# Performance work log

Hardware: AMD Instinct MI355X
Metric: run time of the kernel (lower is better)

Reference implementation:

```python
import jax, jax.numpy as jnp
import numpy as np
from jax import lax


def _na_indices(size, k):
    # NATTEN-style window: window shifts to stay inside the volume.
    centers = np.arange(size)
    start = np.clip(centers - k // 2, 0, size - k)
    idx = start[:, None] + np.arange(k)[None, :]          # (size, k) neighbor coords
    rel = idx - centers[:, None] + (k - 1)                # (size, k) in [0, 2k-2]
    return jnp.asarray(idx), jnp.asarray(rel)


def _ln(x, g, b):
    mu = jnp.mean(x, axis=-1, keepdims=True)
    var = jnp.mean(jnp.square(x - mu), axis=-1, keepdims=True)
    return (x - mu) * lax.rsqrt(var + 1e-5) * g + b


def setup_inputs() -> dict:
    key = jax.random.key(0)
    ks = jax.random.split(key, 12)
    B, C, H, W, Z = 1, 128, 64, 64, 8
    heads, k = 8, 3
    s = lambda kk, shp: (jax.random.normal(kk, shp, jnp.float32) * 0.02)
    return {
        "x": jax.random.normal(ks[0], (B, C, H, W, Z), jnp.float32),
        "ln1_g": jnp.ones((C,), jnp.float32), "ln1_b": jnp.zeros((C,), jnp.float32),
        "qkv_w": s(ks[1], (C, 3 * C)), "qkv_b": jnp.zeros((3 * C,), jnp.float32),
        "proj_w": s(ks[2], (C, C)), "proj_b": jnp.zeros((C,), jnp.float32),
        "rpb": s(ks[3], (heads, 2 * k - 1, 2 * k - 1, 2 * k - 1)),
        "ln2_g": jnp.ones((C,), jnp.float32), "ln2_b": jnp.zeros((C,), jnp.float32),
        "w1": s(ks[4], (C, 4 * C)), "b1": jnp.zeros((4 * C,), jnp.float32),
        "w2": s(ks[5], (4 * C, C)), "b2": jnp.zeros((C,), jnp.float32),
    }


def reference(x, ln1_g, ln1_b, qkv_w, qkv_b, proj_w, proj_b, rpb,
              ln2_g, ln2_b, w1, b1, w2, b2):
    B, C, H, W, Z = x.shape
    heads = rpb.shape[0]
    k = (rpb.shape[1] + 1) // 2
    hd = C // heads
    K3 = k * k * k

    xp = jnp.transpose(x, (0, 2, 3, 4, 1))                 # (B,H,W,Z,C)
    res1 = xp
    xn = _ln(xp, ln1_g, ln1_b)
    qkv = xn @ qkv_w + qkv_b
    q, kk, v = jnp.split(qkv, 3, axis=-1)

    ih, rh = _na_indices(H, k)
    iw, rw = _na_indices(W, k)
    iz, rz = _na_indices(Z, k)
    Ih = ih[:, None, None, :, None, None]
    Iw = iw[None, :, None, None, :, None]
    Iz = iz[None, None, :, None, None, :]
    # gathered neighborhoods: (B,H,W,Z,k,k,k,C) -> (B,H,W,Z,K3,heads,hd)
    k_n = kk[:, Ih, Iw, Iz, :].reshape(B, H, W, Z, K3, heads, hd)
    v_n = v[:, Ih, Iw, Iz, :].reshape(B, H, W, Z, K3, heads, hd)
    qh = q.reshape(B, H, W, Z, heads, hd) * (hd ** -0.5)

    # scores: (B,H,W,Z,heads,K3)
    scores = jnp.einsum('bxyzne,bxyzmne->bxyznm', qh, k_n)
    bias = rpb[:, rh[:, None, None, :, None, None],
                  rw[None, :, None, None, :, None],
                  rz[None, None, :, None, None, :]]        # (heads,H,W,Z,k,k,k)
    bias = bias.reshape(heads, H, W, Z, K3).transpose(1, 2, 3, 0, 4)
    attn = jax.nn.softmax(scores + bias[None], axis=-1)

    out = jnp.einsum('bxyznm,bxyzmne->bxyzne', attn, v_n).reshape(B, H, W, Z, C)
    out = out @ proj_w + proj_b
    x1 = res1 + out                                        # attention residual
    h = jax.nn.gelu(_ln(x1, ln2_g, ln2_b) @ w1 + b1) @ w2 + b2
    x2 = x1 + h                                            # FFN residual

    enc = jnp.transpose(x2, (0, 4, 1, 2, 3))               # (B,C,H,W,Z)
    skip = enc + x                                         # outer residual
    pooled = lax.reduce_window(skip, -jnp.inf, lax.max,
                               (1, 1, 2, 2, 2), (1, 1, 2, 2, 2), 'VALID')
    return (pooled, skip)
```

## Files before the change

### kernel.cpp

```cpp
#include <hip/hip_runtime.h>
#include <hip/hip_bf16.h>
#include <math.h>

#define NPOS 32768

typedef __hip_bfloat16 bf16;
typedef __attribute__((ext_vector_type(8))) short bf16x8;
typedef __attribute__((ext_vector_type(4))) float f32x4;

__device__ __forceinline__ float bf2f(short s) {
    union { unsigned u; float f; } cv;
    cv.u = ((unsigned)(unsigned short)s) << 16;
    return cv.f;
}

__global__ __launch_bounds__(256) void prep_weights_kernel(
    const float* __restrict__ qkv_w, const float* __restrict__ proj_w,
    const float* __restrict__ w1, const float* __restrict__ w2,
    bf16* __restrict__ wt_qkv, bf16* __restrict__ wt_proj,
    bf16* __restrict__ wt_w1, bf16* __restrict__ wt_w2)
{
    int bi = blockIdx.x;
    const float* src; bf16* dst; int K, M, t;
    if (bi < 48)       { src = qkv_w;  dst = wt_qkv;  K = 128; M = 384; t = bi; }
    else if (bi < 64)  { src = proj_w; dst = wt_proj; K = 128; M = 128; t = bi - 48; }
    else if (bi < 128) { src = w1;     dst = wt_w1;   K = 128; M = 512; t = bi - 64; }
    else               { src = w2;     dst = wt_w2;   K = 512; M = 128; t = bi - 128; }
    int tiles_x = M >> 5;
    int m0 = (t % tiles_x) * 32, k0 = (t / tiles_x) * 32;
    __shared__ float tile[32][33];
    int tx = threadIdx.x & 31, ty = threadIdx.x >> 5;
    #pragma unroll
    for (int i = 0; i < 4; i++)
        tile[ty + i * 8][tx] = src[(size_t)(k0 + ty + i * 8) * M + m0 + tx];
    __syncthreads();
    #pragma unroll
    for (int i = 0; i < 4; i++)
        dst[(size_t)(m0 + ty + i * 8) * K + k0 + tx] = __float2bfloat16(tile[tx][ty + i * 8]);
}

__global__ __launch_bounds__(256) void ln1_transpose_kernel(
    const float* __restrict__ x, const float* __restrict__ g,
    const float* __restrict__ b, bf16* __restrict__ out)
{
    __shared__ float tile[128][65];
    __shared__ float red[2][64][4];
    __shared__ float smu[64], srs[64];
    int n0 = blockIdx.x * 64;
    int tid = threadIdx.x;
    #pragma unroll
    for (int i = 0; i < 32; i++) {
        int idx = i * 256 + tid;
        int c = idx >> 6, nn = idx & 63;
        tile[c][nn] = x[(size_t)c * NPOS + n0 + nn];
    }
    __syncthreads();
    {
        int p = tid >> 2, s = tid & 3;
        float sum = 0.f, ssq = 0.f;
        #pragma unroll
        for (int i = 0; i < 32; i++) {
            float v = tile[s * 32 + i][p];
            sum += v; ssq += v * v;
        }
        red[0][p][s] = sum; red[1][p][s] = ssq;
    }
    __syncthreads();
    if (tid < 64) {
        float s = red[0][tid][0] + red[0][tid][1] + red[0][tid][2] + red[0][tid][3];
        float q = red[1][tid][0] + red[1][tid][1] + red[1][tid][2] + red[1][tid][3];
        float mu = s * (1.f / 128.f);
        float var = q * (1.f / 128.f) - mu * mu;
        smu[tid] = mu;
        srs[tid] = rsqrtf(var + 1e-5f);
    }
    __syncthreads();
    #pragma unroll
    for (int i = 0; i < 32; i++) {
        int idx = i * 256 + tid;
        int nn = idx >> 7, c = idx & 127;
        out[(size_t)(n0 + nn) * 128 + c] =
            __float2bfloat16((tile[c][nn] - smu[nn]) * srs[nn] * g[c] + b[c]);
    }
}

__device__ __forceinline__ float gelu_f(float v) {
    float u = 0.7978845608028654f * (v + 0.044715f * v * v * v);
    return v / (1.f + __expf(-2.f * u));
}

template<int MODE, int KT, int BM>
__global__ __launch_bounds__(256) void gemm_mfma_kernel(
    const bf16* __restrict__ A, const bf16* __restrict__ Bt,
    const float* __restrict__ bias, float* __restrict__ outf, bf16* __restrict__ outb,
    bf16* __restrict__ outb2,
    const float* __restrict__ aux0, const bf16* __restrict__ aux1b,
    const float* __restrict__ lng, const float* __restrict__ lnb,
    int N, int M)
{
    constexpr int MF = BM / 32;
    constexpr int NSTEP = KT / 64;
    constexpr int SMEM_BYTES = BM * 144 + 128 * 144;
    __shared__ __align__(16) char smem[SMEM_BYTES];
    bf16 (*As)[72] = (bf16(*)[72])smem;
    bf16 (*Bs)[72] = (bf16(*)[72])(smem + BM * 144);

    int tid = threadIdx.x;
    int row0 = blockIdx.x * BM;
    int col0 = blockIdx.y * 128;
    int lane = tid & 63, wid = tid >> 6;
    int wr = wid >> 1, wc = wid & 1;
    int lr = lane & 15, kg = lane >> 4;

    f32x4 acc[MF][4] = {};
    bf16x8 ra[MF], rb[4];

    #pragma unroll
    for (int i = 0; i < MF; i++) {
        int c = tid + i * 256;
        ra[i] = *(const bf16x8*)(A + (size_t)(row0 + (c >> 3)) * KT + (c & 7) * 8);
    }
    #pragma unroll
    for (int i = 0; i < 4; i++) {
        int c = tid + i * 256;
        rb[i] = *(const bf16x8*)(Bt + (size_t)(col0 + (c >> 3)) * KT + (c & 7) * 8);
    }

    for (int s = 0; s < NSTEP; s++) {
        if (s > 0) __syncthreads();
        #pragma unroll
        for (int i = 0; i < MF; i++) {
            int c = tid + i * 256;
            *(bf16x8*)&As[c >> 3][(c & 7) * 8] = ra[i];
        }
        #pragma unroll
        for (int i = 0; i < 4; i++) {
            int c = tid + i * 256;
            *(bf16x8*)&Bs[c >> 3][(c & 7) * 8] = rb[i];
        }
        __syncthreads();
        if (s + 1 < NSTEP) {
            int k0 = (s + 1) * 64;
            #pragma unroll
            for (int i = 0; i < MF; i++) {
                int c = tid + i * 256;
                ra[i] = *(const bf16x8*)(A + (size_t)(row0 + (c >> 3)) * KT + k0 + (c & 7) * 8);
            }
            #pragma unroll
            for (int i = 0; i < 4; i++) {
                int c = tid + i * 256;
                rb[i] = *(const bf16x8*)(Bt + (size_t)(col0 + (c >> 3)) * KT + k0 + (c & 7) * 8);
            }
        }
        #pragma unroll
        for (int ks = 0; ks < 2; ks++) {
            bf16x8 af[MF], bf_[4];
            #pragma unroll
            for (int m = 0; m < MF; m++)
                af[m] = *(const bf16x8*)&As[wr * (BM / 2) + m * 16 + lr][ks * 32 + kg * 8];
            #pragma unroll
            for (int n = 0; n < 4; n++)
                bf_[n] = *(const bf16x8*)&Bs[wc * 64 + n * 16 + lr][ks * 32 + kg * 8];
            #pragma unroll
            for (int m = 0; m < MF; m++)
                #pragma unroll
                for (int n = 0; n < 4; n++)
                    acc[m][n] = __builtin_amdgcn_mfma_f32_16x16x32_bf16(af[m], bf_[n], acc[m][n], 0, 0, 0);
        }
    }

    if (MODE == 0 || MODE == 2 || MODE == 3) {
        #pragma unroll
        for (int m = 0; m < MF; m++) {
            #pragma unroll
            for (int n = 0; n < 4; n++) {
                int c = col0 + wc * 64 + n * 16 + lr;
                float bv = bias[c];
                #pragma unroll
                for (int j = 0; j < 4; j++) {
                    int r = row0 + wr * (BM / 2) + m * 16 + kg * 4 + j;
                    float v = acc[m][n][j] + bv;
                    if (MODE == 0) {
                        outb[(size_t)r * M + c] = __float2bfloat16(v);
                    } else if (MODE == 2) {
                        outb[(size_t)r * M + c] = __float2bfloat16(gelu_f(v));
                    } else {
                        v += __bfloat162float(aux1b[(size_t)r * 128 + c]) + aux0[(size_t)c * N + r];
                        outf[(size_t)c * N + r] = v;
                    }
                }
            }
        }
    } else {
        __syncthreads();
        float (*rsum)[33] = (float(*)[33])smem;
        float (*rsq)[33]  = (float(*)[33])(smem + 8448);
        float* smu = (float*)(smem + 16896);
        float* srs = (float*)(smem + 17152);
        int slot = wc * 16 + lr;
        #pragma unroll
        for (int m = 0; m < MF; m++) {
            #pragma unroll
            for (int j = 0; j < 4; j++) {
                int rloc = wr * (BM / 2) + m * 16 + kg * 4 + j;
                int r = row0 + rloc;
                float ps = 0.f, pq = 0.f;
                #pragma unroll
                for (int n = 0; n < 4; n++) {
                    int c = wc * 64 + n * 16 + lr;
                    float v = acc[m][n][j] + bias[c] + aux0[(size_t)c * N + r];
                    acc[m][n][j] = v;
                    outb[(size_t)r * 128 + c] = __float2bfloat16(v);
                    ps += v; pq += v * v;
                }
                rsum[rloc][slot] = ps;
                rsq[rloc][slot]  = pq;
            }
        }
        __syncthreads();
        if (tid < 64) {
            float s = 0.f, q = 0.f;
            #pragma unroll
            for (int i = 0; i < 32; i++) { s += rsum[tid][i]; q += rsq[tid][i]; }
            float mu = s * (1.f / 128.f);
            float var = q * (1.f / 128.f) - mu * mu;
            smu[tid] = mu;
            srs[tid] = rsqrtf(var + 1e-5f);
        }
        __syncthreads();
        #pragma unroll
        for (int m = 0; m < MF; m++) {
            #pragma unroll
            for (int j = 0; j < 4; j++) {
                int rloc = wr * (BM / 2) + m * 16 + kg * 4 + j;
                int r = row0 + rloc;
                float mu = smu[rloc], rs = srs[rloc];
                #pragma unroll
                for (int n = 0; n < 4; n++) {
                    int c = wc * 64 + n * 16 + lr;
                    float v = (acc[m][n][j] - mu) * rs * lng[c] + lnb[c];
                    outb2[(size_t)r * 128 + c] = __float2bfloat16(v);
                }
            }
        }
    }
}

__global__ __launch_bounds__(256) void attn_kernel(
    const bf16* __restrict__ qkv,
    const float* __restrict__ rpb,
    bf16* __restrict__ out)
{
    int t = blockIdx.x * 256 + threadIdx.x;
    int head = t & 7, n = t >> 3;
    int z = n & 7, w = (n >> 3) & 63, h = n >> 9;

    int sh = min(max(h - 1, 0), 61);
    int sw = min(max(w - 1, 0), 61);
    int sz = min(max(z - 1, 0), 5);

    float qf[16];
    {
        const bf16* qp = qkv + (size_t)n * 384 + head * 16;
        bf16x8 q0 = *(const bf16x8*)qp;
        bf16x8 q1 = *(const bf16x8*)(qp + 8);
        #pragma unroll
        for (int e = 0; e < 8; e++) {
            qf[e]     = bf2f(q0[e]) * 0.25f;
            qf[e + 8] = bf2f(q1[e]) * 0.25f;
        }
    }

    const bf16*  kbase = qkv + (size_t)((sh << 9) + (sw << 3) + sz) * 384 + 128 + head * 16;
    const float* rp    = rpb + head * 125 + (sh - h + 2) * 25 + (sw - w + 2) * 5 + (sz - z + 2);

    float sc[27];
    float mx = -1e30f;
    #pragma unroll
    for (int a = 0; a < 3; a++) {
        #pragma unroll
        for (int b = 0; b < 3; b++) {
            #pragma unroll
            for (int c = 0; c < 3; c++) {
                const bf16* kp = kbase + (size_t)(a * 512 + b * 8 + c) * 384;
                bf16x8 k0 = *(const bf16x8*)kp;
                bf16x8 k1 = *(const bf16x8*)(kp + 8);
                float s = 0.f;
                #pragma unroll
                for (int e = 0; e < 8; e++) s = fmaf(qf[e], bf2f(k0[e]), s);
                #pragma unroll
                for (int e = 0; e < 8; e++) s = fmaf(qf[e + 8], bf2f(k1[e]), s);
                s += rp[a * 25 + b * 5 + c];
                sc[a * 9 + b * 3 + c] = s;
                mx = fmaxf(mx, s);
            }
        }
    }

    float sum = 0.f;
    #pragma unroll
    for (int m = 0; m < 27; m++) {
        float e = __expf(sc[m] - mx);
        sc[m] = e;
        sum += e;
    }
    float inv = 1.f / sum;

    float o[16] = {};
    #pragma unroll
    for (int a = 0; a < 3; a++) {
        #pragma unroll
        for (int b = 0; b < 3; b++) {
            #pragma unroll
            for (int c = 0; c < 3; c++) {
                const bf16* vp = kbase + (size_t)(a * 512 + b * 8 + c) * 384 + 128;
                bf16x8 v0 = *(const bf16x8*)vp;
                bf16x8 v1 = *(const bf16x8*)(vp + 8);
                float pm = sc[a * 9 + b * 3 + c];
                #pragma unroll
                for (int e = 0; e < 8; e++) {
                    o[e]     = fmaf(pm, bf2f(v0[e]), o[e]);
                    o[e + 8] = fmaf(pm, bf2f(v1[e]), o[e + 8]);
                }
            }
        }
    }

    short os[16];
    #pragma unroll
    for (int e = 0; e < 16; e++) {
        union { bf16 b; short s; } cv;
        cv.b = __float2bfloat16(o[e] * inv);
        os[e] = cv.s;
    }
    bf16* op = out + (size_t)n * 128 + head * 16;
    *(bf16x8*)op       = *(bf16x8*)os;
    *(bf16x8*)(op + 8) = *(bf16x8*)(os + 8);
}

__global__ __launch_bounds__(256) void pool_kernel(
    const float* __restrict__ skip, float* __restrict__ pooled)
{
    int t = blockIdx.x * 256 + threadIdx.x;
    if (t >= 128 * 32 * 32 * 4) return;
    int oz = t & 3, ow = (t >> 2) & 31, oh = (t >> 7) & 31, c = t >> 12;
    const float* base = skip + (size_t)c * 32768 + (oh * 2) * 512 + (ow * 2) * 8 + oz * 2;
    float m = -INFINITY;
    #pragma unroll
    for (int dh = 0; dh < 2; dh++)
        #pragma unroll
        for (int dw = 0; dw < 2; dw++)
            #pragma unroll
            for (int dz = 0; dz < 2; dz++)
                m = fmaxf(m, base[dh * 512 + dw * 8 + dz]);
    pooled[t] = m;
}

extern "C" void kernel_launch(void* const* d_in, const int* in_sizes, int n_in,
                              void* d_out, int out_size, void* d_ws, size_t ws_size,
                              hipStream_t stream) {
    const float* x      = (const float*)d_in[0];
    const float* ln1_g  = (const float*)d_in[1];
    const float* ln1_b  = (const float*)d_in[2];
    const float* qkv_w  = (const float*)d_in[3];
    const float* qkv_b  = (const float*)d_in[4];
    const float* proj_w = (const float*)d_in[5];
    const float* proj_b = (const float*)d_in[6];
    const float* rpb    = (const float*)d_in[7];
    const float* ln2_g  = (const float*)d_in[8];
    const float* ln2_b  = (const float*)d_in[9];
    const float* w1     = (const float*)d_in[10];
    const float* b1     = (const float*)d_in[11];
    const float* w2     = (const float*)d_in[12];
    const float* b2     = (const float*)d_in[13];

    const int N = NPOS;
    char* wsc = (char*)d_ws;
    bf16*  buf0  = (bf16*)wsc;
    bf16*  buf1  = (bf16*)(wsc + (size_t)N * 128 * 2);
    bf16*  buf2b = (bf16*)(wsc + (size_t)N * 128 * 2 + (size_t)N * 512 * 2);
    char*  wts   = wsc + (size_t)N * 128 * 2 + (size_t)N * 512 * 2 + (size_t)N * 128 * 2;
    bf16* wt_qkv  = (bf16*)wts;
    bf16* wt_proj = wt_qkv  + 384 * 128;
    bf16* wt_w1   = wt_proj + 128 * 128;
    bf16* wt_w2   = wt_w1   + 512 * 128;

    float* out_pooled = (float*)d_out;
    float* out_skip   = (float*)d_out + 524288;

    prep_weights_kernel<<<192, 256, 0, stream>>>(qkv_w, proj_w, w1, w2,
                                                 wt_qkv, wt_proj, wt_w1, wt_w2);

    ln1_transpose_kernel<<<N / 64, 256, 0, stream>>>(x, ln1_g, ln1_b, buf0);

    gemm_mfma_kernel<0, 128, 128><<<dim3(N / 128, 3), 256, 0, stream>>>(
        buf0, wt_qkv, qkv_b, nullptr, buf1, nullptr, nullptr, nullptr, nullptr, nullptr, N, 384);

    attn_kernel<<<(N * 8) / 256, 256, 0, stream>>>(buf1, rpb, buf0);

    gemm_mfma_kernel<4, 128, 64><<<dim3(N / 64, 1), 256, 0, stream>>>(
        buf0, wt_proj, proj_b, nullptr, buf2b, buf0, x, nullptr, ln2_g, ln2_b, N, 128);

    gemm_mfma_kernel<2, 128, 128><<<dim3(N / 128, 4), 256, 0, stream>>>(
        buf0, wt_w1, b1, nullptr, buf1, nullptr, nullptr, nullptr, nullptr, nullptr, N, 512);

    gemm_mfma_kernel<3, 512, 64><<<dim3(N / 64, 1), 256, 0, stream>>>(
        buf1, wt_w2, b2, out_skip, nullptr, nullptr, x, buf2b, nullptr, nullptr, N, 128);

    pool_kernel<<<(524288 + 255) / 256, 256, 0, stream>>>(out_skip, out_pooled);
}
```

Measured before the change: 176.0 us.

## Fuse FFN up-projection, GELU and down-projection into one kernel

Replaces the two separate FFN GEMM launches with a single kernel. Each block computes a 32-row hidden tile (GELU of LN2 times W1) in shared memory and immediately multiplies it by W2, then adds the residuals and writes skip. This removes the N x 512 bf16 hidden-activation round trip through global memory and one launch. In exchange, weights are read straight from global memory without shared-memory staging, and the small 32-row tiles cut weight reuse per block.

```diff
diff --git a/kernel.cpp b/kernel.cpp
--- a/kernel.cpp
+++ b/kernel.cpp
@@ -92,9 +92,9 @@
 template<int MODE, int KT, int BM>
 __global__ __launch_bounds__(256) void gemm_mfma_kernel(
     const bf16* __restrict__ A, const bf16* __restrict__ Bt,
-    const float* __restrict__ bias, float* __restrict__ outf, bf16* __restrict__ outb,
+    const float* __restrict__ bias, bf16* __restrict__ outb,
     bf16* __restrict__ outb2,
-    const float* __restrict__ aux0, const bf16* __restrict__ aux1b,
+    const float* __restrict__ aux0,
     const float* __restrict__ lng, const float* __restrict__ lnb,
     int N, int M)
 {
@@ -169,7 +169,7 @@
         }
     }
 
-    if (MODE == 0 || MODE == 2 || MODE == 3) {
+    if (MODE == 0) {
         #pragma unroll
         for (int m = 0; m < MF; m++) {
             #pragma unroll
@@ -179,15 +179,7 @@
                 #pragma unroll
                 for (int j = 0; j < 4; j++) {
                     int r = row0 + wr * (BM / 2) + m * 16 + kg * 4 + j;
-                    float v = acc[m][n][j] + bv;
-                    if (MODE == 0) {
-                        outb[(size_t)r * M + c] = __float2bfloat16(v);
-                    } else if (MODE == 2) {
-                        outb[(size_t)r * M + c] = __float2bfloat16(gelu_f(v));
-                    } else {
-                        v += __bfloat162float(aux1b[(size_t)r * 128 + c]) + aux0[(size_t)c * N + r];
-                        outf[(size_t)c * N + r] = v;
-                    }
+                    outb[(size_t)r * M + c] = __float2bfloat16(acc[m][n][j] + bv);
                 }
             }
         }
@@ -242,6 +234,81 @@
                     outb2[(size_t)r * 128 + c] = __float2bfloat16(v);
                 }
             }
+        }
+    }
+}
+
+__global__ __launch_bounds__(256) void mlp_fused_kernel(
+    const bf16* __restrict__ ln2,
+    const bf16* __restrict__ w1t,
+    const float* __restrict__ b1,
+    const bf16* __restrict__ w2t,
+    const float* __restrict__ b2,
+    const bf16* __restrict__ x1b,
+    const float* __restrict__ x,
+    float* __restrict__ skip,
+    int N)
+{
+    __shared__ __align__(16) bf16 As[32][136];
+    __shared__ __align__(16) bf16 Hs[32][520];
+    int tid = threadIdx.x;
+    int row0 = blockIdx.x * 32;
+    int lane = tid & 63, wid = tid >> 6;
+    int wr = wid >> 1, wc = wid & 1;
+    int lr = lane & 15, kg = lane >> 4;
+
+    #pragma unroll
+    for (int i = 0; i < 2; i++) {
+        int c = tid + i * 256;
+        int r = c >> 4, c16 = c & 15;
+        *(bf16x8*)&As[r][c16 * 8] = *(const bf16x8*)(ln2 + (size_t)(row0 + r) * 128 + c16 * 8);
+    }
+    __syncthreads();
+
+    #pragma unroll
+    for (int cb = 0; cb < 4; cb++) {
+        f32x4 acc[4] = {};
+        #pragma unroll
+        for (int k0 = 0; k0 < 128; k0 += 32) {
+            bf16x8 af = *(const bf16x8*)&As[wr * 16 + lr][k0 + kg * 8];
+            #pragma unroll
+            for (int n = 0; n < 4; n++) {
+                bf16x8 bf_ = *(const bf16x8*)(w1t + (size_t)(cb * 128 + wc * 64 + n * 16 + lr) * 128 + k0 + kg * 8);
+                acc[n] = __builtin_amdgcn_mfma_f32_16x16x32_bf16(af, bf_, acc[n], 0, 0, 0);
+            }
+        }
+        #pragma unroll
+        for (int n = 0; n < 4; n++) {
+            int c = cb * 128 + wc * 64 + n * 16 + lr;
+            float bv = b1[c];
+            #pragma unroll
+            for (int j = 0; j < 4; j++) {
+                int r = wr * 16 + kg * 4 + j;
+                Hs[r][c] = __float2bfloat16(gelu_f(acc[n][j] + bv));
+            }
+        }
+    }
+    __syncthreads();
+
+    f32x4 acc2[4] = {};
+    #pragma unroll
+    for (int k0 = 0; k0 < 512; k0 += 32) {
+        bf16x8 af = *(const bf16x8*)&Hs[wr * 16 + lr][k0 + kg * 8];
+        #pragma unroll
+        for (int n = 0; n < 4; n++) {
+            bf16x8 bf_ = *(const bf16x8*)(w2t + (size_t)(wc * 64 + n * 16 + lr) * 512 + k0 + kg * 8);
+            acc2[n] = __builtin_amdgcn_mfma_f32_16x16x32_bf16(af, bf_, acc2[n], 0, 0, 0);
+        }
+    }
+    #pragma unroll
+    for (int n = 0; n < 4; n++) {
+        int c = wc * 64 + n * 16 + lr;
+        float bv = b2[c];
+        #pragma unroll
+        for (int j = 0; j < 4; j++) {
+            int r = row0 + wr * 16 + kg * 4 + j;
+            float v = acc2[n][j] + bv + __bfloat162float(x1b[(size_t)r * 128 + c]) + x[(size_t)c * N + r];
+            skip[(size_t)c * N + r] = v;
         }
     }
 }
@@ -394,18 +461,15 @@
     ln1_transpose_kernel<<<N / 64, 256, 0, stream>>>(x, ln1_g, ln1_b, buf0);
 
     gemm_mfma_kernel<0, 128, 128><<<dim3(N / 128, 3), 256, 0, stream>>>(
-        buf0, wt_qkv, qkv_b, nullptr, buf1, nullptr, nullptr, nullptr, nullptr, nullptr, N, 384);
+        buf0, wt_qkv, qkv_b, buf1, nullptr, nullptr, nullptr, nullptr, N, 384);
 
     attn_kernel<<<(N * 8) / 256, 256, 0, stream>>>(buf1, rpb, buf0);
 
     gemm_mfma_kernel<4, 128, 64><<<dim3(N / 64, 1), 256, 0, stream>>>(
-        buf0, wt_proj, proj_b, nullptr, buf2b, buf0, x, nullptr, ln2_g, ln2_b, N, 128);
-
-    gemm_mfma_kernel<2, 128, 128><<<dim3(N / 128, 4), 256, 0, stream>>>(
-        buf0, wt_w1, b1, nullptr, buf1, nullptr, nullptr, nullptr, nullptr, nullptr, N, 512);
-
-    gemm_mfma_kernel<3, 512, 64><<<dim3(N / 64, 1), 256, 0, stream>>>(
-        buf1, wt_w2, b2, out_skip, nullptr, nullptr, x, buf2b, nullptr, nullptr, N, 128);
+        buf0, wt_proj, proj_b, buf2b, buf0, x, ln2_g, ln2_b, N, 128);
+
+    mlp_fused_kernel<<<N / 32, 256, 0, stream>>>(
+        buf0, wt_w1, b1, wt_w2, b2, buf2b, x, out_skip, N);
 
     pool_kernel<<<(524288 + 255) / 256, 256, 0, stream>>>(out_skip, out_pooled);
 }
```

Measured after the change: 206.3 us. +17.2%, slower.
